# Kernel optimization log

Hardware: AMD Instinct MI355X
Metric: run time of the kernel (lower is better)

## Reference

```python
import jax, jax.numpy as jnp
import numpy as np

B, D, P, OUT = 16384, 1024, 1024, 25


def setup_inputs() -> dict:
    key = jax.random.key(0)
    ks = jax.random.split(key, 8)
    return {
        "patient_embed": jax.random.normal(ks[0], (B, D), jnp.float32),
        "prototype_embed": jax.random.normal(ks[1], (P, D), jnp.float32),
        "index": jax.random.permutation(ks[2], B),
        "bilinear_w": jax.random.normal(ks[3], (1, D, D), jnp.float32) * 0.02,
        "bilinear_b": jnp.zeros((1,), jnp.float32),
        "lin_w": jax.random.normal(ks[4], (1, 2 * D), jnp.float32) * 0.02,
        "proto_fc_w": jax.random.normal(ks[5], (P, D), jnp.float32) * 0.02,
        "proto_fc_b": jnp.zeros((P,), jnp.float32),
        "class_fc_w": jax.random.normal(ks[6], (OUT, P), jnp.float32) * 0.02,
        "class_fc_b": jnp.zeros((OUT,), jnp.float32),
    }


def reference(patient_embed, prototype_embed, index, bilinear_w, bilinear_b,
              lin_w, proto_fc_w, proto_fc_b, class_fc_w, class_fc_b):
    # prototype codebook is detached in the original (clone().detach())
    protos = jax.lax.stop_gradient(prototype_embed)  # [P, D]

    # cdist + argmin: nearest prototype per patient (VQ-style codebook lookup)
    e_sq = jnp.sum(patient_embed * patient_embed, axis=-1, keepdims=True)  # [B,1]
    p_sq = jnp.sum(protos * protos, axis=-1)[None, :]                      # [1,P]
    d2 = e_sq + p_sq - 2.0 * (patient_embed @ protos.T)                    # [B,P]
    dist = jnp.sqrt(jnp.maximum(d2, 0.0))
    labels_a = jnp.argmin(dist, axis=1)                                    # [B]

    # mixup partner via permutation; its nearest prototype is a gather of labels_a
    embed_b = patient_embed[index]
    labels_b = labels_a[index]

    pa = protos[labels_a]  # [B, D] prototype gather
    pb = protos[labels_b]

    # BiaffineAttention: bilinear(pa, pb) + lin(cat(pa, pb))
    bil = jnp.einsum('bi,oij,bj->bo', pa, bilinear_w, pb) + bilinear_b     # [B,1]
    lin = jnp.concatenate([pa, pb], axis=1) @ lin_w.T                      # [B,1]
    lam = jax.nn.sigmoid(bil + lin)                                        # [B,1]

    # adaptive mixup blend
    mixed_embed = lam * patient_embed + (1.0 - lam) * embed_b              # [B,D]

    # class_linear(mixed_embed) = class_fc(leaky_relu(proto_fc(mixed_embed)))
    proto_logits = mixed_embed @ proto_fc_w.T + proto_fc_b                 # [B,P]
    cls_logits = jax.nn.leaky_relu(proto_logits, 0.01) @ class_fc_w.T + class_fc_b  # [B,OUT]
    return cls_logits
```

## Files before the change

kernel.cpp:

```cpp
#include <hip/hip_runtime.h>
#include <math.h>

#define B_   16384
#define D_   1024
#define P_   1024
#define KS_  2048
#define OUT_ 25
#define NT_  48

typedef unsigned short u16;
typedef unsigned int   u32;
typedef unsigned long long u64;
typedef __attribute__((ext_vector_type(8))) short short8;
typedef __attribute__((ext_vector_type(4))) float f32x4;
typedef _Float16 half_t;
typedef __attribute__((ext_vector_type(2))) _Float16 h2;

struct alignas(8) U16x4 { u16 x, y, z, w; };
struct alignas(8) H4 { half_t x, y, z, w; };
struct alignas(16) H8 { h2 a, b, c, d; };

#if defined(__has_builtin)
#if __has_builtin(__builtin_amdgcn_fdot2)
#define HAS_FDOT2 1
#endif
#endif

#define SBAR()   __builtin_amdgcn_s_barrier()
#define SFENCE() __builtin_amdgcn_sched_barrier(0)
#define WAITV8() asm volatile("s_waitcnt vmcnt(8)" ::: "memory")
#define WAITV0() asm volatile("s_waitcnt vmcnt(0)" ::: "memory")
#define WAITL0() asm volatile("s_waitcnt lgkmcnt(0)" ::: "memory")
#define PRIO1()  __builtin_amdgcn_s_setprio(1)
#define PRIO0()  __builtin_amdgcn_s_setprio(0)

__device__ __forceinline__ u16 f2bf(float f) {
  u32 u = __float_as_uint(f);
  u32 r = (u + 0x7FFFu + ((u >> 16) & 1u)) >> 16;
  return (u16)r;
}
__device__ __forceinline__ float bf2f(u16 h) {
  return __uint_as_float(((u32)h) << 16);
}
__device__ __forceinline__ u32 ordkey(float f) {
  u32 u = __float_as_uint(f);
  return (u & 0x80000000u) ? ~u : (u | 0x80000000u);
}
__device__ __forceinline__ void gload_lds16(const u16* g, u16* l) {
  __builtin_amdgcn_global_load_lds(
      (const __attribute__((address_space(1))) u32*)g,
      (__attribute__((address_space(3))) u32*)l, 16, 0, 0);
}
__device__ __forceinline__ float dot8(const H8& a, const H8& b, float c) {
#ifdef HAS_FDOT2
  c = __builtin_amdgcn_fdot2(a.a, b.a, c, false);
  c = __builtin_amdgcn_fdot2(a.b, b.b, c, false);
  c = __builtin_amdgcn_fdot2(a.c, b.c, c, false);
  c = __builtin_amdgcn_fdot2(a.d, b.d, c, false);
#else
  c += (float)a.a.x * (float)b.a.x + (float)a.a.y * (float)b.a.y;
  c += (float)a.b.x * (float)b.b.x + (float)a.b.y * (float)b.b.y;
  c += (float)a.c.x * (float)b.c.x + (float)a.c.y * (float)b.c.y;
  c += (float)a.d.x * (float)b.d.x + (float)a.d.y * (float)b.d.y;
#endif
  return c;
}
__device__ __forceinline__ int wrapNT(int t) { return t >= NT_ ? t - NT_ : t; }
__device__ __forceinline__ int acolf(int t) { t = wrapNT(t); return ((t >> 4) == 1 ? 1024 : 0) + (t & 15) * 64; }
__device__ __forceinline__ int bcolf(int t) { t = wrapNT(t); return ((t >> 4) == 2 ? 1024 : 0) + (t & 15) * 64; }


__global__ void conv_split(const float* __restrict__ in, u16* __restrict__ out) {
  int r = blockIdx.x, t = threadIdx.x;
  float4 x = ((const float4*)(in + (size_t)r * D_))[t];
  U16x4 h, l;
  h.x = f2bf(x.x); l.x = f2bf(x.x - bf2f(h.x));
  h.y = f2bf(x.y); l.y = f2bf(x.y - bf2f(h.y));
  h.z = f2bf(x.z); l.z = f2bf(x.z - bf2f(h.z));
  h.w = f2bf(x.w); l.w = f2bf(x.w - bf2f(h.w));
  u16* o = out + (size_t)r * KS_ + t * 4;
  *(U16x4*)(o)      = h;
  *(U16x4*)(o + D_) = l;
}

__global__ void convProtos(const float* __restrict__ protos, const float* __restrict__ lin_w,
                           u16* __restrict__ p2,
                           float* __restrict__ psq, float* __restrict__ uu, float* __restrict__ vv) {
  int r = blockIdx.x, t = threadIdx.x;
  float4 x  = ((const float4*)(protos + (size_t)r * D_))[t];
  float4 w1 = ((const float4*)(lin_w))[t];
  float4 w2 = ((const float4*)(lin_w + D_))[t];
  U16x4 h, l;
  h.x = f2bf(x.x); l.x = f2bf(x.x - bf2f(h.x));
  h.y = f2bf(x.y); l.y = f2bf(x.y - bf2f(h.y));
  h.z = f2bf(x.z); l.z = f2bf(x.z - bf2f(h.z));
  h.w = f2bf(x.w); l.w = f2bf(x.w - bf2f(h.w));
  u16* o = p2 + (size_t)r * KS_ + t * 4;
  *(U16x4*)(o) = h; *(U16x4*)(o + D_) = l;

  float s1 = x.x*x.x + x.y*x.y + x.z*x.z + x.w*x.w;
  float s2 = x.x*w1.x + x.y*w1.y + x.z*w1.z + x.w*w1.w;
  float s3 = x.x*w2.x + x.y*w2.y + x.z*w2.z + x.w*w2.w;
  #pragma unroll
  for (int mk = 1; mk < 64; mk <<= 1) {
    s1 += __shfl_xor(s1, mk);
    s2 += __shfl_xor(s2, mk);
    s3 += __shfl_xor(s3, mk);
  }
  __shared__ float r1[4], r2[4], r3[4];
  if ((t & 63) == 0) { int w = t >> 6; r1[w] = s1; r2[w] = s2; r3[w] = s3; }
  __syncthreads();
  if (t == 0) {
    psq[r] = r1[0] + r1[1] + r1[2] + r1[3];
    uu[r]  = r2[0] + r2[1] + r2[2] + r2[3];
    vv[r]  = r3[0] + r3[1] + r3[2] + r3[3];
  }
}

__global__ void convWt(const float* __restrict__ W, u16* __restrict__ wt2) {
  __shared__ float tile[64][65];
  int bx = blockIdx.x, by = blockIdx.y;
  int t = threadIdx.x;
  int c4 = (t & 15) * 4, r0 = t >> 4;
  #pragma unroll
  for (int rr = 0; rr < 64; rr += 16) {
    int r = rr + r0;
    float4 x = *(const float4*)(W + (size_t)(bx * 64 + r) * D_ + by * 64 + c4);
    tile[r][c4 + 0] = x.x; tile[r][c4 + 1] = x.y; tile[r][c4 + 2] = x.z; tile[r][c4 + 3] = x.w;
  }
  __syncthreads();
  #pragma unroll
  for (int rr = 0; rr < 64; rr += 16) {
    int r = rr + r0;
    U16x4 h, l;
    float v0 = tile[c4 + 0][r], v1 = tile[c4 + 1][r], v2 = tile[c4 + 2][r], v3 = tile[c4 + 3][r];
    h.x = f2bf(v0); l.x = f2bf(v0 - bf2f(h.x));
    h.y = f2bf(v1); l.y = f2bf(v1 - bf2f(h.y));
    h.z = f2bf(v2); l.z = f2bf(v2 - bf2f(h.z));
    h.w = f2bf(v3); l.w = f2bf(v3 - bf2f(h.w));
    u16* o = wt2 + (size_t)(by * 64 + r) * KS_ + bx * 64 + c4;
    *(U16x4*)(o) = h; *(U16x4*)(o + D_) = l;
  }
}

#define MFMAQ(MH, AF, BQ)                                                        \
  {                                                                              \
    _Pragma("unroll")                                                            \
    for (int mi = 0; mi < 4; ++mi) {                                             \
      _Pragma("unroll")                                                          \
      for (int nj = 0; nj < 4; ++nj)                                             \
        acc[(MH) * 4 + mi][nj] = __builtin_amdgcn_mfma_f32_16x16x32_bf16(        \
            (AF)[mi], (BQ)[nj], acc[(MH) * 4 + mi][nj], 0, 0, 0);                \
    }                                                                            \
  }

template<int MODE>
__global__ __launch_bounds__(512, 2) void gemm256(
    const u16* __restrict__ A, const u16* __restrict__ Bm,
    u16* __restrict__ Ch,
    const float* __restrict__ psq, u64* __restrict__ packed,
    const float* __restrict__ bias)
{
  extern __shared__ u16 lds[];
  int bid = blockIdx.x;
  int wg = ((bid & 7) << 5) + (bid >> 3);
  int tm = wg >> 2, tn = wg & 3;
  int m0 = tm << 8, n0 = tn << 8;

  int tid = threadIdx.x;
  int w = tid >> 6, lane = tid & 63;
  int wm = w >> 2, wn = w & 3;
  int lr = lane & 15, lg = lane >> 4;

  #define AOFF(kkh, buf) (((kkh) * 2 + (buf)) * 8192)
  #define BOFF(kkh, buf) (32768 + ((kkh) * 2 + (buf)) * 8192)

  auto stage = [&](const u16* src, int row0, int colbase, int dstoff) {
    #pragma unroll
    for (int q = 0; q < 2; ++q) {
      int r = q * 128 + w * 16 + (lane >> 2);
      int c = ((lane & 3) * 8) ^ (((r >> 3) & 1) << 4);
      gload_lds16(src + (size_t)(row0 + r) * KS_ + colbase + c,
                  &lds[dstoff + q * 4096 + w * 512]);
    }
  };
  auto lda = [&](int kkh, int buf, int mh, short8* dst) {
    const u16* Asl = &lds[AOFF(kkh, buf)];
    #pragma unroll
    for (int mi = 0; mi < 4; ++mi) {
      int r = wm * 128 + mh * 64 + mi * 16 + lr;
      dst[mi] = *(const short8*)&Asl[r * 32 + ((lg * 8) ^ (((r >> 3) & 1) << 4))];
    }
  };
  auto ldb = [&](int kkh, int buf, short8* dst) {
    const u16* Bsl = &lds[BOFF(kkh, buf)];
    #pragma unroll
    for (int nj = 0; nj < 4; ++nj) {
      int r = wn * 64 + nj * 16 + lr;
      dst[nj] = *(const short8*)&Bsl[r * 32 + ((lg * 8) ^ (((r >> 3) & 1) << 4))];
    }
  };

  stage(A,  m0, acolf(0) +  0, AOFF(0, 0));
  stage(A,  m0, acolf(0) + 32, AOFF(1, 0));
  stage(Bm, n0, bcolf(0) +  0, BOFF(0, 0));
  stage(Bm, n0, bcolf(0) + 32, BOFF(1, 0));

  f32x4 acc[8][4];
  #pragma unroll
  for (int i = 0; i < 8; ++i)
    #pragma unroll
    for (int j = 0; j < 4; ++j)
      acc[i][j] = (f32x4){0.f, 0.f, 0.f, 0.f};

  short8 af[4], bq[4];
  for (int t = 0; t < NT_; ++t) {
    int buf = t & 1, nbuf = buf ^ 1;
    stage(A,  m0, acolf(t + 1) +  0, AOFF(0, nbuf));
    stage(A,  m0, acolf(t + 1) + 32, AOFF(1, nbuf));
    stage(Bm, n0, bcolf(t + 1) +  0, BOFF(0, nbuf));
    stage(Bm, n0, bcolf(t + 1) + 32, BOFF(1, nbuf));
    WAITV8();
    SBAR();
    lda(0, buf, 0, af); ldb(0, buf, bq);
    WAITL0(); SFENCE();
    PRIO1(); MFMAQ(0, af, bq); PRIO0(); SFENCE();
    lda(0, buf, 1, af);
    WAITL0(); SFENCE();
    PRIO1(); MFMAQ(1, af, bq); PRIO0(); SFENCE();
    lda(1, buf, 0, af); ldb(1, buf, bq);
    WAITL0(); SFENCE();
    PRIO1(); MFMAQ(0, af, bq); PRIO0(); SFENCE();
    lda(1, buf, 1, af);
    WAITL0(); SFENCE();
    PRIO1(); MFMAQ(1, af, bq); PRIO0(); SFENCE();
    SBAR();
  }
  WAITV0();

  if (MODE == 1) {
    float pq[4];
    #pragma unroll
    for (int nj = 0; nj < 4; ++nj) pq[nj] = psq[n0 + wn * 64 + nj * 16 + lr];
    #pragma unroll
    for (int mi = 0; mi < 8; ++mi) {
      #pragma unroll
      for (int r = 0; r < 4; ++r) {
        float best = 1e30f; int bestn = 0x7fffffff;
        #pragma unroll
        for (int nj = 0; nj < 4; ++nj) {
          int n = n0 + wn * 64 + nj * 16 + lr;
          float d = pq[nj] - 2.0f * acc[mi][nj][r];
          if (d < best || (d == best && n < bestn)) { best = d; bestn = n; }
        }
        #pragma unroll
        for (int mk = 1; mk < 16; mk <<= 1) {
          float od = __shfl_xor(best, mk);
          int   on = __shfl_xor(bestn, mk);
          if (od < best || (od == best && on < bestn)) { best = od; bestn = on; }
        }
        if (lr == 0) {
          int m = m0 + wm * 128 + mi * 16 + lg * 4 + r;
          u64 key = ((u64)ordkey(best) << 32) | (u32)bestn;
          atomicMin(&packed[m], key);
        }
      }
    }
  } else {
    float bc[4];
    #pragma unroll
    for (int nj = 0; nj < 4; ++nj) bc[nj] = bias[n0 + wn * 64 + nj * 16 + lr];
    #pragma unroll
    for (int mi = 0; mi < 8; ++mi)
      #pragma unroll
      for (int nj = 0; nj < 4; ++nj)
        #pragma unroll
        for (int r = 0; r < 4; ++r) {
          int m = m0 + wm * 128 + mi * 16 + lg * 4 + r;
          int n = n0 + wn * 64 + nj * 16 + lr;
          float val = acc[mi][nj][r] + bc[nj];
          val = val >= 0.f ? val : 0.01f * val;
          half_t hv = (half_t)val;
          Ch[(size_t)m * P_ + n] = __builtin_bit_cast(u16, hv);
        }
  }
  #undef AOFF
  #undef BOFF
}

__global__ __launch_bounds__(256) void gemm_T_splitk(
    const u16* __restrict__ A, const u16* __restrict__ Bm, float* __restrict__ Cp)
{
  __shared__ u16 As[128 * 32];
  __shared__ u16 Bs[128 * 32];

  int bid = blockIdx.x;
  int swz = (bid & 7) * 24 + (bid >> 3);
  int kp = swz >> 6;
  int wg = swz & 63;
  int tm = wg >> 3, tn = wg & 7;
  int m0 = tm * 128, n0 = tn * 128;
  int abase = (kp == 1) ? 1024 : 0;
  int bbase = (kp == 2) ? 1024 : 0;

  int t = threadIdx.x;
  int w = t >> 6, lane = t & 63;
  int wr = w >> 1, wc = w & 1;
  int lr = lane & 15, lg = lane >> 4;

  const u16* src = (w < 2) ? A : Bm;
  int base_row = (w < 2) ? m0 : n0;
  int kbase = (w < 2) ? abase : bbase;
  int half = w & 1;
  int srow = base_row + half * 64 + (lane >> 2);
  int scol = (lane & 3) * 8;
  const u16* gsrc = src + (size_t)srow * KS_ + kbase + scol;
  u16* lbase = ((w < 2) ? As : Bs) + half * 2048;

  f32x4 acc[4][4];
  #pragma unroll
  for (int i = 0; i < 4; ++i)
    #pragma unroll
    for (int j = 0; j < 4; ++j)
      acc[i][j] = (f32x4){0.f, 0.f, 0.f, 0.f};

  for (int kt = 0; kt < 32; ++kt) {
    #pragma unroll
    for (int p = 0; p < 4; ++p)
      gload_lds16(gsrc + kt * 32 + (size_t)p * 16 * KS_, lbase + p * 512);
    __syncthreads();
    short8 af[4], bfr[4];
    #pragma unroll
    for (int i = 0; i < 4; ++i)
      af[i] = *(const short8*)&As[(wr * 64 + i * 16 + lr) * 32 + lg * 8];
    #pragma unroll
    for (int j = 0; j < 4; ++j)
      bfr[j] = *(const short8*)&Bs[(wc * 64 + j * 16 + lr) * 32 + lg * 8];
    #pragma unroll
    for (int i = 0; i < 4; ++i)
      #pragma unroll
      for (int j = 0; j < 4; ++j)
        acc[i][j] = __builtin_amdgcn_mfma_f32_16x16x32_bf16(af[i], bfr[j], acc[i][j], 0, 0, 0);
    __syncthreads();
  }

  float* Co = Cp + (size_t)kp * (P_ * D_);
  #pragma unroll
  for (int i = 0; i < 4; ++i)
    #pragma unroll
    for (int j = 0; j < 4; ++j)
      #pragma unroll
      for (int r = 0; r < 4; ++r) {
        int m = m0 + wr * 64 + i * 16 + lg * 4 + r;
        int n = n0 + wc * 64 + j * 16 + lr;
        Co[(size_t)m * D_ + n] = acc[i][j][r];
      }
}

__global__ void mix_kernel(const u64* __restrict__ packed, const int* __restrict__ index,
                           const float* __restrict__ Tp, const float* __restrict__ protos,
                           const float* __restrict__ patient,
                           const float* __restrict__ uu, const float* __restrict__ vv,
                           const float* __restrict__ bilb, u16* __restrict__ mixed2)
{
  int b = blockIdx.x, t = threadIdx.x;
  int la = (int)(packed[b] & 0xffffffffULL);
  int ib = index[b];
  int lb = (int)(packed[ib] & 0xffffffffULL);

  float4 t0 = ((const float4*)(Tp + (size_t)la * D_))[t];
  float4 t1 = ((const float4*)(Tp + (size_t)(P_ * D_) + (size_t)la * D_))[t];
  float4 t2 = ((const float4*)(Tp + (size_t)(2 * P_ * D_) + (size_t)la * D_))[t];
  float4 pb = ((const float4*)(protos + (size_t)lb * D_))[t];
  float tax = t0.x + t1.x + t2.x, tay = t0.y + t1.y + t2.y;
  float taz = t0.z + t1.z + t2.z, taw = t0.w + t1.w + t2.w;
  float part = tax*pb.x + tay*pb.y + taz*pb.z + taw*pb.w;
  #pragma unroll
  for (int mk = 1; mk < 64; mk <<= 1) part += __shfl_xor(part, mk);
  __shared__ float ws4[4];
  __shared__ float lamsh;
  if ((t & 63) == 0) ws4[t >> 6] = part;
  __syncthreads();
  if (t == 0) {
    float dot = ws4[0] + ws4[1] + ws4[2] + ws4[3];
    float z = dot + bilb[0] + uu[la] + vv[lb];
    lamsh = 1.0f / (1.0f + expf(-z));
  }
  __syncthreads();
  float lam = lamsh, oml = 1.0f - lam;

  float4 xa = ((const float4*)(patient + (size_t)b  * D_))[t];
  float4 xb = ((const float4*)(patient + (size_t)ib * D_))[t];
  float m0v = lam * xa.x + oml * xb.x;
  float m1v = lam * xa.y + oml * xb.y;
  float m2v = lam * xa.z + oml * xb.z;
  float m3v = lam * xa.w + oml * xb.w;
  U16x4 h, l;
  h.x = f2bf(m0v); l.x = f2bf(m0v - bf2f(h.x));
  h.y = f2bf(m1v); l.y = f2bf(m1v - bf2f(h.y));
  h.z = f2bf(m2v); l.z = f2bf(m2v - bf2f(h.z));
  h.w = f2bf(m3v); l.w = f2bf(m3v - bf2f(h.w));
  u16* o = mixed2 + (size_t)b * KS_ + t * 4;
  *(U16x4*)(o) = h; *(U16x4*)(o + D_) = l;
}

__global__ __launch_bounds__(256) void cls_kernel(const u16* __restrict__ pl,
                                                  const float* __restrict__ w,
                                                  const float* __restrict__ bias,
                                                  float* __restrict__ out)
{
  __shared__ half_t wl[25 * 1032];
  int t = threadIdx.x;
  for (int i = t; i < 25 * 256; i += 256) {
    float4 v = ((const float4*)w)[i];
    int o = i >> 8;
    int col = (i & 255) * 4;
    H4 hh; hh.x = (half_t)v.x; hh.y = (half_t)v.y; hh.z = (half_t)v.z; hh.w = (half_t)v.w;
    *(H4*)&wl[o * 1032 + col] = hh;
  }
  __syncthreads();

  int row = blockIdx.x * 64 + (t >> 2);
  int osub = t & 3;
  const H8* prow = (const H8*)(pl + (size_t)row * P_);
  float acc[7] = {0.f, 0.f, 0.f, 0.f, 0.f, 0.f, 0.f};

  for (int kk = 0; kk < 128; ++kk) {
    H8 a = prow[kk];
    #pragma unroll
    for (int j = 0; j < 7; ++j) {
      int o = 4 * j + osub;
      if (o < 25) {
        H8 wv = *(const H8*)&wl[o * 1032 + kk * 8];
        acc[j] = dot8(a, wv, acc[j]);
      }
    }
  }
  #pragma unroll
  for (int j = 0; j < 7; ++j) {
    int o = 4 * j + osub;
    if (o < 25) out[(size_t)row * OUT_ + o] = acc[j] + bias[o];
  }
}

extern "C" void kernel_launch(void* const* d_in, const int* in_sizes, int n_in,
                              void* d_out, int out_size, void* d_ws, size_t ws_size,
                              hipStream_t stream)
{
  const float* patient = (const float*)d_in[0];
  const float* protos  = (const float*)d_in[1];
  const int*   index   = (const int*)d_in[2];
  const float* W       = (const float*)d_in[3];
  const float* bilb    = (const float*)d_in[4];
  const float* lin_w   = (const float*)d_in[5];
  const float* pfc_w   = (const float*)d_in[6];
  const float* pfc_b   = (const float*)d_in[7];
  const float* cls_w   = (const float*)d_in[8];
  const float* cls_b   = (const float*)d_in[9];
  float* out = (float*)d_out;

  char* ws = (char*)d_ws;
  size_t off = 0;
  auto carve = [&](size_t bytes) -> char* {
    char* p = ws + off; off += (bytes + 255) & ~(size_t)255; return p;
  };
  u16* buf2   = (u16*)carve((size_t)B_ * KS_ * 2);
  u16* plh    = (u16*)carve((size_t)B_ * P_ * 2);
  u16* p2     = (u16*)carve((size_t)P_ * KS_ * 2);
  u16* pfc2   = (u16*)carve((size_t)P_ * KS_ * 2);
  u16* wt2    = (u16*)carve((size_t)D_ * KS_ * 2);
  float* Tp   = (float*)carve((size_t)3 * P_ * D_ * 4);
  u64* packed = (u64*)carve((size_t)B_ * 8);
  float* psq  = (float*)carve(P_ * 4);
  float* uu   = (float*)carve(P_ * 4);
  float* vv   = (float*)carve(P_ * 4);

  hipMemsetAsync(packed, 0xFF, (size_t)B_ * 8, stream);

  convProtos<<<P_, 256, 0, stream>>>(protos, lin_w, p2, psq, uu, vv);
  convWt<<<dim3(16, 16), 256, 0, stream>>>(W, wt2);
  conv_split<<<P_, 256, 0, stream>>>(pfc_w, pfc2);
  conv_split<<<B_, 256, 0, stream>>>(patient, buf2);

  gemm_T_splitk<<<192, 256, 0, stream>>>(p2, wt2, Tp);
  gemm256<1><<<256, 512, 131072, stream>>>(buf2, p2, nullptr, psq, packed, nullptr);
  mix_kernel<<<B_, 256, 0, stream>>>(packed, index, Tp, protos, patient, uu, vv, bilb, buf2);
  gemm256<2><<<256, 512, 131072, stream>>>(buf2, pfc2, plh, nullptr, nullptr, pfc_b);
  cls_kernel<<<256, 256, 0, stream>>>(plh, cls_w, cls_b, out);
}
```

Baseline: 442.8 us.

## Load GEMM B operand directly from global into registers, halve LDS

```diff
diff --git a/kernel.cpp b/kernel.cpp
--- a/kernel.cpp
+++ b/kernel.cpp
@@ -27,10 +27,7 @@
 #endif
 
 #define SBAR()   __builtin_amdgcn_s_barrier()
-#define SFENCE() __builtin_amdgcn_sched_barrier(0)
-#define WAITV8() asm volatile("s_waitcnt vmcnt(8)" ::: "memory")
 #define WAITV0() asm volatile("s_waitcnt vmcnt(0)" ::: "memory")
-#define WAITL0() asm volatile("s_waitcnt lgkmcnt(0)" ::: "memory")
 #define PRIO1()  __builtin_amdgcn_s_setprio(1)
 #define PRIO0()  __builtin_amdgcn_s_setprio(0)
 
@@ -143,14 +140,14 @@
   }
 }
 
-#define MFMAQ(MH, AF, BQ)                                                        \
+#define MFMAQ(MH, AF, BQ, O)                                                     \
   {                                                                              \
     _Pragma("unroll")                                                            \
     for (int mi = 0; mi < 4; ++mi) {                                             \
       _Pragma("unroll")                                                          \
       for (int nj = 0; nj < 4; ++nj)                                             \
         acc[(MH) * 4 + mi][nj] = __builtin_amdgcn_mfma_f32_16x16x32_bf16(        \
-            (AF)[mi], (BQ)[nj], acc[(MH) * 4 + mi][nj], 0, 0, 0);                \
+            (AF)[mi], (BQ)[(O) + nj], acc[(MH) * 4 + mi][nj], 0, 0, 0);          \
     }                                                                            \
   }
 
@@ -173,14 +170,13 @@
   int lr = lane & 15, lg = lane >> 4;
 
   #define AOFF(kkh, buf) (((kkh) * 2 + (buf)) * 8192)
-  #define BOFF(kkh, buf) (32768 + ((kkh) * 2 + (buf)) * 8192)
-
-  auto stage = [&](const u16* src, int row0, int colbase, int dstoff) {
+
+  auto stage = [&](int row0, int colbase, int dstoff) {
     #pragma unroll
     for (int q = 0; q < 2; ++q) {
       int r = q * 128 + w * 16 + (lane >> 2);
       int c = ((lane & 3) * 8) ^ (((r >> 3) & 1) << 4);
-      gload_lds16(src + (size_t)(row0 + r) * KS_ + colbase + c,
+      gload_lds16(A + (size_t)(row0 + r) * KS_ + colbase + c,
                   &lds[dstoff + q * 4096 + w * 512]);
     }
   };
@@ -192,19 +188,16 @@
       dst[mi] = *(const short8*)&Asl[r * 32 + ((lg * 8) ^ (((r >> 3) & 1) << 4))];
     }
   };
-  auto ldb = [&](int kkh, int buf, short8* dst) {
-    const u16* Bsl = &lds[BOFF(kkh, buf)];
-    #pragma unroll
-    for (int nj = 0; nj < 4; ++nj) {
-      int r = wn * 64 + nj * 16 + lr;
-      dst[nj] = *(const short8*)&Bsl[r * 32 + ((lg * 8) ^ (((r >> 3) & 1) << 4))];
-    }
+  const u16* browbase = Bm + (size_t)(n0 + wn * 64 + lr) * KS_ + lg * 8;
+  auto loadB = [&](int t, short8* dst) {
+    int cb = bcolf(t);
+    #pragma unroll
+    for (int kkh = 0; kkh < 2; ++kkh)
+      #pragma unroll
+      for (int nj = 0; nj < 4; ++nj)
+        dst[kkh * 4 + nj] =
+            *(const short8*)(browbase + (size_t)(nj * 16) * KS_ + cb + kkh * 32);
   };
-
-  stage(A,  m0, acolf(0) +  0, AOFF(0, 0));
-  stage(A,  m0, acolf(0) + 32, AOFF(1, 0));
-  stage(Bm, n0, bcolf(0) +  0, BOFF(0, 0));
-  stage(Bm, n0, bcolf(0) + 32, BOFF(1, 0));
 
   f32x4 acc[8][4];
   #pragma unroll
@@ -213,30 +206,35 @@
     for (int j = 0; j < 4; ++j)
       acc[i][j] = (f32x4){0.f, 0.f, 0.f, 0.f};
 
-  short8 af[4], bq[4];
-  for (int t = 0; t < NT_; ++t) {
-    int buf = t & 1, nbuf = buf ^ 1;
-    stage(A,  m0, acolf(t + 1) +  0, AOFF(0, nbuf));
-    stage(A,  m0, acolf(t + 1) + 32, AOFF(1, nbuf));
-    stage(Bm, n0, bcolf(t + 1) +  0, BOFF(0, nbuf));
-    stage(Bm, n0, bcolf(t + 1) + 32, BOFF(1, nbuf));
-    WAITV8();
-    SBAR();
-    lda(0, buf, 0, af); ldb(0, buf, bq);
-    WAITL0(); SFENCE();
-    PRIO1(); MFMAQ(0, af, bq); PRIO0(); SFENCE();
-    lda(0, buf, 1, af);
-    WAITL0(); SFENCE();
-    PRIO1(); MFMAQ(1, af, bq); PRIO0(); SFENCE();
-    lda(1, buf, 0, af); ldb(1, buf, bq);
-    WAITL0(); SFENCE();
-    PRIO1(); MFMAQ(0, af, bq); PRIO0(); SFENCE();
-    lda(1, buf, 1, af);
-    WAITL0(); SFENCE();
-    PRIO1(); MFMAQ(1, af, bq); PRIO0(); SFENCE();
-    SBAR();
-  }
+  short8 af[4], bqA[8], bqB[8];
+
+  stage(m0, acolf(0) +  0, AOFF(0, 0));
+  stage(m0, acolf(0) + 32, AOFF(1, 0));
+  loadB(0, bqA);
   WAITV0();
+
+  #define TILEBODY(T, BUF, NBUF, BQC, BQN)                                      \
+  {                                                                             \
+    SBAR();                                                                     \
+    stage(m0, acolf((T) + 1) +  0, AOFF(0, NBUF));                              \
+    stage(m0, acolf((T) + 1) + 32, AOFF(1, NBUF));                              \
+    loadB((T) + 1, BQN);                                                        \
+    lda(0, BUF, 0, af);                                                         \
+    PRIO1(); MFMAQ(0, af, BQC, 0); PRIO0();                                     \
+    lda(0, BUF, 1, af);                                                         \
+    PRIO1(); MFMAQ(1, af, BQC, 0); PRIO0();                                     \
+    lda(1, BUF, 0, af);                                                         \
+    PRIO1(); MFMAQ(0, af, BQC, 4); PRIO0();                                     \
+    lda(1, BUF, 1, af);                                                         \
+    PRIO1(); MFMAQ(1, af, BQC, 4); PRIO0();                                     \
+    WAITV0();                                                                   \
+  }
+
+  for (int t = 0; t < NT_; t += 2) {
+    TILEBODY(t,     0, 1, bqA, bqB);
+    TILEBODY(t + 1, 1, 0, bqB, bqA);
+  }
+  #undef TILEBODY
 
   if (MODE == 1) {
     float pq[4];
@@ -285,7 +283,6 @@
         }
   }
   #undef AOFF
-  #undef BOFF
 }
 
 __global__ __launch_bounds__(256) void gemm_T_splitk(
@@ -483,8 +480,8 @@
   conv_split<<<B_, 256, 0, stream>>>(patient, buf2);
 
   gemm_T_splitk<<<192, 256, 0, stream>>>(p2, wt2, Tp);
-  gemm256<1><<<256, 512, 131072, stream>>>(buf2, p2, nullptr, psq, packed, nullptr);
+  gemm256<1><<<256, 512, 65536, stream>>>(buf2, p2, nullptr, psq, packed, nullptr);
   mix_kernel<<<B_, 256, 0, stream>>>(packed, index, Tp, protos, patient, uu, vv, bilb, buf2);
-  gemm256<2><<<256, 512, 131072, stream>>>(buf2, pfc2, plh, nullptr, nullptr, pfc_b);
+  gemm256<2><<<256, 512, 65536, stream>>>(buf2, pfc2, plh, nullptr, nullptr, pfc_b);
   cls_kernel<<<256, 256, 0, stream>>>(plh, cls_w, cls_b, out);
 }
```

New measurement: 534.8 us. 20.8% more time.
